# Kernel optimization log

Hardware: AMD Instinct MI355X
Metric: run time of the kernel (lower is better)

## Reference

```python
import jax, jax.numpy as jnp
import numpy as np

N_HEAD = 16
N_EMBD = 1024
B, T = 4, 1024


def setup_inputs() -> dict:
    key = jax.random.key(0)
    ks = jax.random.split(key, 8)
    hs = N_EMBD // N_HEAD
    x = jax.random.normal(ks[0], (B, T, N_EMBD), dtype=jnp.float32)
    # previous-layer attention load per token, ~O(1/T) like a softmax column mean
    refractory_state = jax.random.uniform(ks[1], (B, T), dtype=jnp.float32) / T
    s_attn = 1.0 / np.sqrt(N_EMBD)
    W_attn = jax.random.normal(ks[2], (N_EMBD, 3 * N_EMBD), dtype=jnp.float32) * s_attn
    b_attn = jnp.zeros((3 * N_EMBD,), dtype=jnp.float32)
    W_proj = jax.random.normal(ks[3], (N_EMBD, N_EMBD), dtype=jnp.float32) * s_attn
    b_proj = jnp.zeros((N_EMBD,), dtype=jnp.float32)
    # learnable LIF params, init per module (lif_mode='refractory')
    threshold = jnp.full((N_HEAD,), 0.01, dtype=jnp.float32)
    leak = jnp.full((N_HEAD,), 2.0, dtype=jnp.float32)
    steepness = jnp.full((N_HEAD,), 2.0, dtype=jnp.float32)
    ref_strength = jnp.full((N_HEAD,), -2.0, dtype=jnp.float32)
    cross_w = jnp.full((N_HEAD,), -2.0, dtype=jnp.float32)
    return {
        "x": x, "refractory_state": refractory_state,
        "W_attn": W_attn, "b_attn": b_attn,
        "W_proj": W_proj, "b_proj": b_proj,
        "threshold": threshold, "leak": leak, "steepness": steepness,
        "ref_strength": ref_strength, "cross_w": cross_w,
    }


def reference(x, refractory_state, W_attn, b_attn, W_proj, b_proj,
              threshold, leak, steepness, ref_strength, cross_w):
    Bq, Tq, C = x.shape
    H = N_HEAD
    hs = C // H
    qkv = x @ W_attn + b_attn                     # [B,T,3C]
    q, k, v = jnp.split(qkv, 3, axis=-1)
    q = q.reshape(Bq, Tq, H, hs).transpose(0, 2, 1, 3)  # [B,H,T,hs]
    k = k.reshape(Bq, Tq, H, hs).transpose(0, 2, 1, 3)
    v = v.reshape(Bq, Tq, H, hs).transpose(0, 2, 1, 3)

    att = jnp.einsum('bhqd,bhkd->bhqk', q, k) * (1.0 / jnp.sqrt(jnp.asarray(hs, x.dtype)))
    causal = jnp.tril(jnp.ones((Tq, Tq), dtype=bool))
    att = jnp.where(causal[None, None], att, -jnp.inf)
    probs = jax.nn.softmax(att, axis=-1)          # [B,H,T,T]

    thr = (jnp.abs(threshold) * 0.1)[None, :, None, None]
    lk = jax.nn.sigmoid(leak)[None, :, None, None]
    st = jax.nn.softplus(steepness)[None, :, None, None]
    # refractory: column load over queries + cross-layer load
    column_load = probs.mean(axis=-2, keepdims=True)          # [B,H,1,T]
    eff_thr = thr + jax.nn.softplus(ref_strength)[None, :, None, None] * column_load
    eff_thr = eff_thr + jax.nn.sigmoid(cross_w)[None, :, None, None] * refractory_state[:, None, None, :]

    fire = jax.nn.sigmoid(st * (probs - eff_thr))
    lif_w = fire + lk * (1.0 - fire)
    mod = probs * lif_w
    mod = mod / (mod.sum(axis=-1, keepdims=True) + 1e-8)
    new_refractory = mod.mean(axis=1).mean(axis=-2)           # [B,T]

    y = jnp.einsum('bhqk,bhkd->bhqd', mod, v)
    y = y.transpose(0, 2, 1, 3).reshape(Bq, Tq, C)
    y = y @ W_proj + b_proj
    return y, new_refractory
```

## Files before the change

kernel.cpp:

```cpp
#include <hip/hip_runtime.h>
#include <math.h>

#define B_  4
#define T_  1024
#define C_  1024
#define H_  16
#define HS_ 64
#define K2E 0.1803368801f
#define LOG2E 1.44269504f

typedef _Float16 f16;
typedef _Float16 f16x8 __attribute__((ext_vector_type(8)));
typedef _Float16 f16x4 __attribute__((ext_vector_type(4)));
typedef float f32x4 __attribute__((ext_vector_type(4)));

#define MFMA16(a,b,c) __builtin_amdgcn_mfma_f32_16x16x32_f16(a,b,c,0,0,0)
#define EXP2(x) __builtin_amdgcn_exp2f(x)
#define RCP(x)  __builtin_amdgcn_rcpf(x)

#define PSTRIDE_BH 557056

__device__ __forceinline__ float qsum_(float v){
    v += __shfl_xor(v,1,64); v += __shfl_xor(v,2,64);
    v += __shfl_xor(v,4,64); v += __shfl_xor(v,8,64);
    return v;
}
__device__ __forceinline__ float sigmoidf_(float x){ return 1.0f/(1.0f + __expf(-x)); }
__device__ __forceinline__ float softplusf_(float x){ return fmaxf(x, 0.0f) + log1pf(__expf(-fabsf(x))); }

__device__ __forceinline__ void gload_lds16(const f16* g, f16* l){
    __builtin_amdgcn_global_load_lds(
        (__attribute__((address_space(1))) void*)(void*)g,
        (__attribute__((address_space(3))) void*)(void*)l, 16, 0, 0);
}

__global__ __launch_bounds__(256) void prep_k(
    const float* __restrict__ x, const float* __restrict__ Wa,
    const float* __restrict__ Wp,
    f16* __restrict__ x_h, f16* __restrict__ WaT, f16* __restrict__ WpT,
    float* __restrict__ zbase)
{
    __shared__ float tl[32][33];
    const int bid = blockIdx.x, tid = threadIdx.x;
    if (bid < 2048){
        int i = bid*256 + tid;
        const float4* p = (const float4*)x + (size_t)i*2;
        float4 a = p[0], b = p[1];
        f16x8 o;
        o[0]=(f16)a.x; o[1]=(f16)a.y; o[2]=(f16)a.z; o[3]=(f16)a.w;
        o[4]=(f16)b.x; o[5]=(f16)b.y; o[6]=(f16)b.z; o[7]=(f16)b.w;
        *((f16x8*)x_h + i) = o;
    } else if (bid < 5120){
        int t = bid - 2048;
        int n0 = (t % 96)*32, k0 = (t / 96)*32;
        const int c = tid & 31, r4 = tid >> 5;
        #pragma unroll
        for (int i=0;i<4;i++){ int r = r4*4+i; tl[r][c] = Wa[(size_t)(k0+r)*3072 + n0 + c]; }
        __syncthreads();
        #pragma unroll
        for (int i=0;i<4;i++){ int r = r4*4+i; WaT[(size_t)(n0+r)*1024 + k0 + c] = (f16)tl[c][r]; }
    } else if (bid < 6144){
        int t = bid - 5120;
        int n0 = (t & 31)*32, k0 = (t >> 5)*32;
        const int c = tid & 31, r4 = tid >> 5;
        #pragma unroll
        for (int i=0;i<4;i++){ int r = r4*4+i; tl[r][c] = Wp[(size_t)(k0+r)*1024 + n0 + c]; }
        __syncthreads();
        #pragma unroll
        for (int i=0;i<4;i++){ int r = r4*4+i; WpT[(size_t)(n0+r)*1024 + k0 + c] = (f16)tl[c][r]; }
    } else {
        int idx = (bid - 6144)*256 + tid;
        float4 z; z.x=0.f; z.y=0.f; z.z=0.f; z.w=0.f;
        ((float4*)zbase)[idx] = z;
    }
}

#define CT_STRIDE 132
__global__ __launch_bounds__(256) void gemm_qkv_k(
    const f16* __restrict__ A, const f16* __restrict__ Bt,
    const float* __restrict__ bias,
    f16* __restrict__ Qh, f16* __restrict__ Kh, f16* __restrict__ Vt)
{
    __shared__ __align__(16) f16 smem[16896];
    const int tid = threadIdx.x;
    const int lane = tid & 63, wave = tid >> 6;
    const int lx = lane & 15, quad = lane >> 4;
    const int wm = wave & 1, wn = wave >> 1;
    const int lin = blockIdx.y*24 + blockIdx.x;
    const int nb  = (lin & 7)*96 + (lin >> 3);
    const int m0 = (nb/24)*128, n0 = (nb%24)*128;
    const f16* Ap = A  + (size_t)m0*1024;
    const f16* Bp = Bt + (size_t)n0*1024;
    f32x4 acc[4][4];
    #pragma unroll
    for (int i=0;i<4;i++){
        #pragma unroll
        for (int j=0;j<4;j++){ acc[i][j][0]=0.f;acc[i][j][1]=0.f;acc[i][j][2]=0.f;acc[i][j][3]=0.f; }
    }
#define GQ_STAGE(BUF, KT) { \
    const int k0s = (KT)*32; \
    for (int i=0;i<2;i++){ int c=i*4+wave; \
        gload_lds16(Ap + (size_t)(c*16+lx)*1024 + k0s + quad*8, &smem[(BUF) + c*512]); \
        gload_lds16(Bp + (size_t)(c*16+lx)*1024 + k0s + quad*8, &smem[(BUF) + 4096 + c*512]); } }
#define GQ_COMP(BUF) { \
    f16x8 af[4], bf[4]; \
    for (int mt=0;mt<4;mt++) af[mt] = *(const f16x8*)&smem[(BUF) + (wm*4+mt)*512 + quad*128 + lx*8]; \
    for (int nt=0;nt<4;nt++) bf[nt] = *(const f16x8*)&smem[(BUF) + 4096 + (wn*4+nt)*512 + quad*128 + lx*8]; \
    for (int mt=0;mt<4;mt++) \
        for (int nt=0;nt<4;nt++) \
            acc[mt][nt] = MFMA16(af[mt], bf[nt], acc[mt][nt]); }

    GQ_STAGE(0, 0);
    __syncthreads();
    #pragma unroll 1
    for (int it=0; it<32; it+=2){
        if (it+1 < 32) GQ_STAGE(8192, it+1);
        GQ_COMP(0);
        __syncthreads();
        if (it+2 < 32) GQ_STAGE(0, it+2);
        GQ_COMP(8192);
        __syncthreads();
    }
    f16* Ct = smem;
    #pragma unroll
    for (int mt=0;mt<4;mt++){
        #pragma unroll
        for (int nt=0;nt<4;nt++){
            int n_loc = wn*64 + nt*16 + lx;
            float bv = bias[n0 + n_loc];
            #pragma unroll
            for (int r=0;r<4;r++){
                int m_loc = wm*64 + mt*16 + quad*4 + r;
                Ct[m_loc*CT_STRIDE + n_loc] = (f16)(acc[mt][nt][r] + bv);
            }
        }
    }
    __syncthreads();
    const int bb = m0 >> 10;
    if (n0 < 2048){
        for (int it=0; it<8; it++){
            int row = it*32 + wave*8 + (lane>>3);
            int ch  = lane & 7;
            int m_loc = row >> 1, half = row & 1;
            f16x8 v = *(const f16x8*)&Ct[m_loc*CT_STRIDE + half*64 + ch*8];
            int n = n0 + half*64;
            int which = n >> 10, cc = n & 1023, h = cc >> 6;
            int t = (m0 + m_loc) & 1023;
            f16* dst = (which==0) ? Qh : Kh;
            *(f16x8*)(dst + ((size_t)(bb*16+h)*1024 + t)*64 + ch*8) = v;
        }
    } else {
        for (int it=0; it<8; it++){
            int drow = it*16 + wave*4 + (lane>>4);
            int ch   = lane & 15;
            int cc = (n0 + drow) & 1023;
            int h = cc >> 6, d = cc & 63;
            f16 tmp[8];
            #pragma unroll
            for (int j=0;j<8;j++) tmp[j] = Ct[(ch*8+j)*CT_STRIDE + drow];
            int t = (m0 + ch*8) & 1023;
            *(f16x8*)(Vt + ((size_t)(bb*16+h)*64 + d)*1024 + t) = *(f16x8*)tmp;
        }
    }
}

__global__ __launch_bounds__(256) void gemm_proj_k(
    const f16* __restrict__ A, const f16* __restrict__ Bt,
    const float* __restrict__ bias, float* __restrict__ out,
    const float* __restrict__ racc)
{
    if (blockIdx.x == 512){
        float* oref = out + (size_t)B_*T_*C_;
        #pragma unroll
        for (int j=0;j<16;j++){
            int idx = j*256 + threadIdx.x;
            oref[idx] = racc[idx] * (1.0f/(H_*T_));
        }
        return;
    }
    __shared__ __align__(16) f16 smem[12288];
    const int tid = threadIdx.x;
    const int lane = tid & 63, wave = tid >> 6;
    const int lx = lane & 15, quad = lane >> 4;
    const int wm = wave & 1, wn = wave >> 1;
    const int lin = blockIdx.x;
    const int nb  = (lin & 7)*64 + (lin >> 3);
    const int m0 = (nb >> 4)*128, n0 = (nb & 15)*64;
    const f16* Ap = A  + (size_t)m0*1024;
    const f16* Bp = Bt + (size_t)n0*1024;
    f32x4 acc[4][2];
    #pragma unroll
    for (int i=0;i<4;i++){
        #pragma unroll
        for (int j=0;j<2;j++){ acc[i][j][0]=0.f;acc[i][j][1]=0.f;acc[i][j][2]=0.f;acc[i][j][3]=0.f; }
    }
#define GP_STAGE(BUF, KT) { \
    const int k0s = (KT)*32; \
    for (int i=0;i<2;i++){ int c=i*4+wave; \
        gload_lds16(Ap + (size_t)(c*16+lx)*1024 + k0s + quad*8, &smem[(BUF) + c*512]); } \
    gload_lds16(Bp + (size_t)(wave*16+lx)*1024 + k0s + quad*8, &smem[(BUF) + 4096 + wave*512]); }
#define GP_COMP(BUF) { \
    f16x8 af[4], bf[2]; \
    for (int mt=0;mt<4;mt++) af[mt] = *(const f16x8*)&smem[(BUF) + (wm*4+mt)*512 + quad*128 + lx*8]; \
    for (int nt=0;nt<2;nt++) bf[nt] = *(const f16x8*)&smem[(BUF) + 4096 + (wn*2+nt)*512 + quad*128 + lx*8]; \
    for (int mt=0;mt<4;mt++) \
        for (int nt=0;nt<2;nt++) \
            acc[mt][nt] = MFMA16(af[mt], bf[nt], acc[mt][nt]); }

    GP_STAGE(0, 0);
    __syncthreads();
    #pragma unroll 1
    for (int it=0; it<32; it+=2){
        if (it+1 < 32) GP_STAGE(6144, it+1);
        GP_COMP(0);
        __syncthreads();
        if (it+2 < 32) GP_STAGE(0, it+2);
        GP_COMP(6144);
        __syncthreads();
    }
    #pragma unroll
    for (int mt=0;mt<4;mt++){
        #pragma unroll
        for (int nt=0;nt<2;nt++){
            int n = n0 + wn*32 + nt*16 + lx;
            float bv = bias[n];
            #pragma unroll
            for (int r=0;r<4;r++){
                int m = m0 + wm*64 + mt*16 + quad*4 + r;
                out[(size_t)m*1024 + n] = acc[mt][nt][r] + bv;
            }
        }
    }
}

__global__ __launch_bounds__(256) void attn_stats_k(
    const f16* __restrict__ Qh, const f16* __restrict__ Kh,
    float* __restrict__ rowl, float* __restrict__ colp,
    f16* __restrict__ Pbuf)
{
    __shared__ __align__(16) f16 Kl[8192];
    __shared__ __align__(16) f16 Pl[4][16*72];
    __shared__ float invl_sh[64];
    const int tid = threadIdx.x;
    const int lane = tid & 63, wave = tid >> 6;
    const int lx = lane & 15, quad = lane >> 4;
    const int g  = 15 - (blockIdx.x >> 6);
    const int bh = blockIdx.x & 63;
    const int qpos = wave*16 + quad*4;
    const size_t kbase = (size_t)bh*65536;
    const int S = (g+1)*64;
    f16* __restrict__ Pblk = Pbuf + (size_t)bh*PSTRIDE_BH + (size_t)4096*((g*(g+1))>>1);

    const size_t qoff = ((size_t)bh*1024 + g*64 + wave*16 + lx)*64;
    f16x8 aq0 = *(const f16x8*)(Qh + qoff + quad*8);
    f16x8 aq1 = *(const f16x8*)(Qh + qoff + 32 + quad*8);

#define KLOAD(dst, KT) { \
    for (int i=0;i<2;i++){ int u=i*4+wave, cc=u&3, kh=u>>2; \
        dst[i] = *(const f16x8*)(Kh + kbase + (size_t)((KT)*64 + cc*16+lx)*64 + kh*32 + quad*8); } }
#define KSTORE(src, BUF) { \
    for (int i=0;i<2;i++){ int u=i*4+wave, cc=u&3, kh=u>>2; \
        *(f16x8*)&Kl[(BUF) + cc*1024 + kh*512 + quad*128 + lx*8] = src[i]; } }
#define STATS1_TILE(KT, BUF) { \
    const bool diag = ((KT) == g); \
    for (int nt=0;nt<4;nt++){ \
        f32x4 sc = {0.f,0.f,0.f,0.f}; \
        f16x8 b0 = *(const f16x8*)&Kl[(BUF) + nt*1024 + quad*128 + lx*8]; \
        f16x8 b1 = *(const f16x8*)&Kl[(BUF) + nt*1024 + 512 + quad*128 + lx*8]; \
        sc = MFMA16(aq0, b0, sc); \
        sc = MFMA16(aq1, b1, sc); \
        for (int r=0;r<4;r++){ \
            float sv = sc[r]; \
            if (diag && (nt*16+lx) > (qpos + r)) sv = -1e4f; \
            float p = EXP2(sv*K2E); \
            ls[r] += p; \
            Pl[wave][(quad*4+r)*72 + nt*16 + lx] = (f16)p; \
        } } \
    for (int it2=0; it2<2; it2++){ \
        int qq = it2*8 + (lane>>3), chh = lane & 7; \
        f16x8 v = *(const f16x8*)&Pl[wave][qq*72 + chh*8]; \
        *(f16x8*)(Pblk + (size_t)(wave*16+qq)*S + (KT)*64 + chh*8) = v; } }

    f16x8 rkE[2], rkO[2];
    float ls[4] = {0.f,0.f,0.f,0.f};
    KLOAD(rkE, 0);
    KSTORE(rkE, 0);
    if (g >= 1) KLOAD(rkO, 1);
    __syncthreads();
    #pragma unroll 1
    for (int kt=0; kt<=g; kt+=2){
        if (kt+2 <= g) KLOAD(rkE, kt+2);
        if (kt+1 <= g) KSTORE(rkO, 4096);
        STATS1_TILE(kt, 0);
        __syncthreads();
        if (kt+1 <= g){
            if (kt+3 <= g) KLOAD(rkO, kt+3);
            if (kt+2 <= g) KSTORE(rkE, 0);
            STATS1_TILE(kt+1, 4096);
            __syncthreads();
        }
    }
    #pragma unroll
    for (int r=0;r<4;r++){
        float l = qsum_(ls[r]);
        if (lx == 0){
            rowl[(size_t)bh*1024 + g*64 + qpos + r] = l;
            invl_sh[qpos + r] = RCP(l);
        }
    }
    __syncthreads();
    if (tid < (g+1)*16){
        const int k0 = tid*4;
        float a0=0.f, a1=0.f, a2=0.f, a3=0.f;
        const f16* pr = Pblk + k0;
        #pragma unroll 4
        for (int q=0;q<64;q++){
            f16x4 v = *(const f16x4*)(pr + (size_t)q*S);
            float w = invl_sh[q];
            a0 += (float)v[0]*w; a1 += (float)v[1]*w;
            a2 += (float)v[2]*w; a3 += (float)v[3]*w;
        }
        float* cp = colp + (size_t)bh*1024 + k0;
        atomicAdd(cp+0,a0); atomicAdd(cp+1,a1);
        atomicAdd(cp+2,a2); atomicAdd(cp+3,a3);
    }
}

__global__ __launch_bounds__(256) void attn_apply_k(
    const f16* __restrict__ Vt,
    const float* __restrict__ rowl,
    const float* __restrict__ colp, const float* __restrict__ refr,
    const float* __restrict__ threshold, const float* __restrict__ leak,
    const float* __restrict__ steepness, const float* __restrict__ ref_strength,
    const float* __restrict__ cross_w,
    f16* __restrict__ Yh, float* __restrict__ racc,
    f16* __restrict__ Pbuf)
{
    __shared__ __align__(16) f16 Pl[4][16*72];
    __shared__ float eb[1024];
    __shared__ float invl_sh[64];
    __shared__ float invD_sh[64];
    const int tid = threadIdx.x;
    const int lane = tid & 63, wave = tid >> 6;
    const int lx = lane & 15, quad = lane >> 4;
    const int g  = 15 - (blockIdx.x >> 6);
    const int bh = blockIdx.x & 63;
    const int b  = bh >> 4, h = bh & 15;
    const size_t kbase = (size_t)bh*65536;
    const int S = (g+1)*64;
    f16* __restrict__ Pblk = Pbuf + (size_t)bh*PSTRIDE_BH + (size_t)4096*((g*(g+1))>>1);

    const float thr = fabsf(threshold[h])*0.1f;
    const float lk  = sigmoidf_(leak[h]);
    const float st2 = softplusf_(steepness[h]) * LOG2E;
    const float sprT= softplusf_(ref_strength[h]) * (1.0f/T_);
    const float cw  = sigmoidf_(cross_w[h]);
    const float Alk = 1.f - lk;

    {
        float4 cp = *(const float4*)(colp + (size_t)bh*1024 + tid*4);
        float4 rf = *(const float4*)(refr + (size_t)b*1024 + tid*4);
        eb[tid*4+0] = st2*(thr + sprT*cp.x + cw*rf.x);
        eb[tid*4+1] = st2*(thr + sprT*cp.y + cw*rf.y);
        eb[tid*4+2] = st2*(thr + sprT*cp.z + cw*rf.z);
        eb[tid*4+3] = st2*(thr + sprT*cp.w + cw*rf.w);
    }
    if (tid < 64) invl_sh[tid] = RCP(rowl[(size_t)bh*1024 + g*64 + tid]);
    __syncthreads();

    const float wli = invl_sh[wave*16 + lx];

    f32x4 y[4];
    #pragma unroll
    for (int i=0;i<4;i++){ y[i][0]=0.f;y[i][1]=0.f;y[i][2]=0.f;y[i][3]=0.f; }
    float Dp = 0.f;

#define PLOADX(dst, KT) { \
    const f16* pp = Pblk + (size_t)(wave*16 + lx)*S + (KT)*64 + quad*8; \
    dst[0] = *(const f16x8*)(pp); \
    dst[1] = *(const f16x8*)(pp + 32); }
#define RVLOAD(dst, KT) { \
    for (int dt=0;dt<4;dt++){ \
        const f16* vp = Vt + kbase + (size_t)(dt*16 + lx)*1024 + (KT)*64 + quad*8; \
        dst[dt*2]   = *(const f16x8*)(vp); \
        dst[dt*2+1] = *(const f16x8*)(vp + 32); } }
#define LIF_TILE(KT, pv, af0, af1) { \
    const float* ebp = &eb[(KT)*64 + quad*8]; \
    float4 eA0 = *(const float4*)(ebp); \
    float4 eA1 = *(const float4*)(ebp+4); \
    float4 eB0 = *(const float4*)(ebp+32); \
    float4 eB1 = *(const float4*)(ebp+36); \
    float ea[8] = {eA0.x,eA0.y,eA0.z,eA0.w,eA1.x,eA1.y,eA1.z,eA1.w}; \
    float ebb[8] = {eB0.x,eB0.y,eB0.z,eB0.w,eB1.x,eB1.y,eB1.z,eB1.w}; \
    for (int jj=0;jj<8;jj++){ \
        float p = (float)pv[0][jj] * wli; \
        float fire = RCP(1.f + EXP2(ea[jj] - st2*p)); \
        float pw = p*(lk + Alk*fire); \
        Dp += pw; af0[jj] = (f16)pw; } \
    for (int jj=0;jj<8;jj++){ \
        float p = (float)pv[1][jj] * wli; \
        float fire = RCP(1.f + EXP2(ebb[jj] - st2*p)); \
        float pw = p*(lk + Alk*fire); \
        Dp += pw; af1[jj] = (f16)pw; } }
#define MFMA8(af0, af1, rv) { \
    __builtin_amdgcn_s_setprio(1); \
    for (int dt=0;dt<4;dt++){ \
        y[dt] = MFMA16(af0, rv[dt*2],   y[dt]); \
        y[dt] = MFMA16(af1, rv[dt*2+1], y[dt]); } \
    __builtin_amdgcn_s_setprio(0); }

    f16x8 rvA[8], rvB[8], pvA[2], pvB[2], af0, af1;
    PLOADX(pvA, 0); RVLOAD(rvA, 0);
    if (g >= 1){ PLOADX(pvB, 1); RVLOAD(rvB, 1); }
    #pragma unroll 1
    for (int kt=0; kt<=g; kt+=2){
        LIF_TILE(kt, pvA, af0, af1);
        if (kt+2 <= g) PLOADX(pvA, kt+2);
        MFMA8(af0, af1, rvA);
        if (kt+2 <= g) RVLOAD(rvA, kt+2);
        if (kt+1 <= g){
            LIF_TILE(kt+1, pvB, af0, af1);
            if (kt+3 <= g) PLOADX(pvB, kt+3);
            MFMA8(af0, af1, rvB);
            if (kt+3 <= g) RVLOAD(rvB, kt+3);
        }
    }
    Dp += __shfl_xor(Dp,16,64); Dp += __shfl_xor(Dp,32,64);
    float invDl = RCP(Dp + 1e-8f);
    if (quad == 0) invD_sh[wave*16 + lx] = invDl;

    float invD[4];
    #pragma unroll
    for (int r=0;r<4;r++) invD[r] = invD_sh[wave*16 + quad*4 + r];
    #pragma unroll
    for (int dt=0;dt<4;dt++){
        #pragma unroll
        for (int r=0;r<4;r++)
            Pl[wave][(quad*4+r)*72 + dt*16 + lx] = (f16)(y[dt][r]*invD[r]);
    }
    #pragma unroll
    for (int it=0; it<2; it++){
        int q = it*8 + (lane>>3), ch = lane & 7;
        f16x8 v = *(const f16x8*)&Pl[wave][q*72 + ch*8];
        *(f16x8*)(Yh + (size_t)(b*1024 + g*64 + wave*16 + q)*1024 + h*64 + ch*8) = v;
    }

    __syncthreads();

    if (tid < (g+1)*16){
        const int k0 = tid*4;
        float4 ebv = *(const float4*)&eb[k0];
        float a0=0.f, a1=0.f, a2=0.f, a3=0.f;
        const f16* pr = Pblk + k0;
        #pragma unroll 4
        for (int q=0;q<64;q++){
            f16x4 v = *(const f16x4*)(pr + (size_t)q*S);
            float wl = invl_sh[q], wd = invD_sh[q];
            float p0 = (float)v[0]*wl, p1 = (float)v[1]*wl;
            float p2 = (float)v[2]*wl, p3 = (float)v[3]*wl;
            float f0 = RCP(1.f + EXP2(ebv.x - st2*p0));
            float f1 = RCP(1.f + EXP2(ebv.y - st2*p1));
            float f2 = RCP(1.f + EXP2(ebv.z - st2*p2));
            float f3 = RCP(1.f + EXP2(ebv.w - st2*p3));
            a0 += p0*(lk + Alk*f0)*wd; a1 += p1*(lk + Alk*f1)*wd;
            a2 += p2*(lk + Alk*f2)*wd; a3 += p3*(lk + Alk*f3)*wd;
        }
        float* rp = racc + (size_t)b*1024 + k0;
        atomicAdd(rp+0,a0); atomicAdd(rp+1,a1);
        atomicAdd(rp+2,a2); atomicAdd(rp+3,a3);
    }
}

extern "C" void kernel_launch(void* const* d_in, const int* in_sizes, int n_in,
                              void* d_out, int out_size, void* d_ws, size_t ws_size,
                              hipStream_t stream) {
    (void)in_sizes; (void)n_in; (void)out_size; (void)ws_size;
    const float* x           = (const float*)d_in[0];
    const float* refr        = (const float*)d_in[1];
    const float* W_attn      = (const float*)d_in[2];
    const float* b_attn      = (const float*)d_in[3];
    const float* W_proj      = (const float*)d_in[4];
    const float* b_proj      = (const float*)d_in[5];
    const float* threshold   = (const float*)d_in[6];
    const float* leak        = (const float*)d_in[7];
    const float* steepness   = (const float*)d_in[8];
    const float* ref_strength= (const float*)d_in[9];
    const float* cross_w     = (const float*)d_in[10];
    float* out = (float*)d_out;

    char* ws = (char*)d_ws;
    f16* x_h = (f16*)ws;                       ws += (size_t)4096*1024*2;
    f16* WaT = (f16*)ws;                       ws += (size_t)3072*1024*2;
    f16* WpT = (f16*)ws;                       ws += (size_t)1024*1024*2;
    f16* Qh  = (f16*)ws;                       ws += (size_t)64*1024*64*2;
    f16* Kh  = (f16*)ws;                       ws += (size_t)64*1024*64*2;
    f16* Vt  = (f16*)ws;                       ws += (size_t)64*64*1024*2;
    f16* Yh  = (f16*)ws;                       ws += (size_t)4096*1024*2;
    float* rowl = (float*)ws;                  ws += (size_t)65536*4;
    float* colp = (float*)ws;                  ws += (size_t)65536*4;
    float* racc = (float*)ws;                  ws += (size_t)4096*4;
    f16* Pbuf = (f16*)ws;                      ws += (size_t)64*PSTRIDE_BH*2;

    prep_k<<<dim3(6212), dim3(256), 0, stream>>>(x, W_attn, W_proj, x_h, WaT, WpT, colp);
    gemm_qkv_k<<<dim3(24,32), dim3(256), 0, stream>>>(x_h, WaT, b_attn, Qh, Kh, Vt);
    attn_stats_k<<<dim3(1024), dim3(256), 0, stream>>>(Qh, Kh, rowl, colp, Pbuf);
    attn_apply_k<<<dim3(1024), dim3(256), 0, stream>>>(
        Vt, rowl, colp, refr,
        threshold, leak, steepness, ref_strength, cross_w, Yh, racc, Pbuf);
    gemm_proj_k<<<dim3(513), dim3(256), 0, stream>>>(Yh, WpT, b_proj, out, racc);
}
```

Measured before the change: 277.0 us.

## Stage V tiles in shared memory once per block instead of per-wave global loads

The attention-apply kernel previously had each of the four waves load the full 64x64 V tile from global memory into registers. Now each wave loads a quarter of the tile, writes it into a double-buffered LDS array, and all waves read their MFMA B operands from LDS. This cuts redundant global/L2 traffic for V by four and reduces register pressure. In exchange it adds __syncthreads barriers per tile and LDS read traffic, and it drops the setprio hints around the MFMAs.

```diff
diff --git a/kernel.cpp b/kernel.cpp
--- a/kernel.cpp
+++ b/kernel.cpp
@@ -336,6 +336,7 @@
     f16* __restrict__ Yh, float* __restrict__ racc,
     f16* __restrict__ Pbuf)
 {
+    __shared__ __align__(16) f16 Vl[8192];
     __shared__ __align__(16) f16 Pl[4][16*72];
     __shared__ float eb[1024];
     __shared__ float invl_sh[64];
@@ -375,16 +376,17 @@
     for (int i=0;i<4;i++){ y[i][0]=0.f;y[i][1]=0.f;y[i][2]=0.f;y[i][3]=0.f; }
     float Dp = 0.f;
 
+#define VLOAD(dst, KT) { \
+    for (int i=0;i<2;i++){ int u=i*4+wave, cc=u&3, kh=u>>2; \
+        dst[i] = *(const f16x8*)(Vt + kbase + (size_t)(cc*16+lx)*1024 + (KT)*64 + kh*32 + quad*8); } }
+#define VSTORE(src, BUF) { \
+    for (int i=0;i<2;i++){ int u=i*4+wave, cc=u&3, kh=u>>2; \
+        *(f16x8*)&Vl[(BUF) + cc*1024 + kh*512 + quad*128 + lx*8] = src[i]; } }
 #define PLOADX(dst, KT) { \
     const f16* pp = Pblk + (size_t)(wave*16 + lx)*S + (KT)*64 + quad*8; \
     dst[0] = *(const f16x8*)(pp); \
     dst[1] = *(const f16x8*)(pp + 32); }
-#define RVLOAD(dst, KT) { \
-    for (int dt=0;dt<4;dt++){ \
-        const f16* vp = Vt + kbase + (size_t)(dt*16 + lx)*1024 + (KT)*64 + quad*8; \
-        dst[dt*2]   = *(const f16x8*)(vp); \
-        dst[dt*2+1] = *(const f16x8*)(vp + 32); } }
-#define LIF_TILE(KT, pv, af0, af1) { \
+#define APPLY_T(KT, BUF, pv) { \
     const float* ebp = &eb[(KT)*64 + quad*8]; \
     float4 eA0 = *(const float4*)(ebp); \
     float4 eA1 = *(const float4*)(ebp+4); \
@@ -392,6 +394,7 @@
     float4 eB1 = *(const float4*)(ebp+36); \
     float ea[8] = {eA0.x,eA0.y,eA0.z,eA0.w,eA1.x,eA1.y,eA1.z,eA1.w}; \
     float ebb[8] = {eB0.x,eB0.y,eB0.z,eB0.w,eB1.x,eB1.y,eB1.z,eB1.w}; \
+    f16x8 af0, af1; \
     for (int jj=0;jj<8;jj++){ \
         float p = (float)pv[0][jj] * wli; \
         float fire = RCP(1.f + EXP2(ea[jj] - st2*p)); \
@@ -401,33 +404,35 @@
         float p = (float)pv[1][jj] * wli; \
         float fire = RCP(1.f + EXP2(ebb[jj] - st2*p)); \
         float pw = p*(lk + Alk*fire); \
-        Dp += pw; af1[jj] = (f16)pw; } }
-#define MFMA8(af0, af1, rv) { \
-    __builtin_amdgcn_s_setprio(1); \
+        Dp += pw; af1[jj] = (f16)pw; } \
     for (int dt=0;dt<4;dt++){ \
-        y[dt] = MFMA16(af0, rv[dt*2],   y[dt]); \
-        y[dt] = MFMA16(af1, rv[dt*2+1], y[dt]); } \
-    __builtin_amdgcn_s_setprio(0); }
-
-    f16x8 rvA[8], rvB[8], pvA[2], pvB[2], af0, af1;
-    PLOADX(pvA, 0); RVLOAD(rvA, 0);
-    if (g >= 1){ PLOADX(pvB, 1); RVLOAD(rvB, 1); }
+        f16x8 bv0 = *(const f16x8*)&Vl[(BUF) + dt*1024 + quad*128 + lx*8]; \
+        f16x8 bv1 = *(const f16x8*)&Vl[(BUF) + dt*1024 + 512 + quad*128 + lx*8]; \
+        y[dt] = MFMA16(af0, bv0, y[dt]); \
+        y[dt] = MFMA16(af1, bv1, y[dt]); } }
+
+    f16x8 rvE[2], rvO[2], pvE[2], pvO[2];
+    VLOAD(rvE, 0); PLOADX(pvE, 0);
+    VSTORE(rvE, 0);
+    if (g >= 1){ VLOAD(rvO, 1); PLOADX(pvO, 1); }
+    __syncthreads();
     #pragma unroll 1
     for (int kt=0; kt<=g; kt+=2){
-        LIF_TILE(kt, pvA, af0, af1);
-        if (kt+2 <= g) PLOADX(pvA, kt+2);
-        MFMA8(af0, af1, rvA);
-        if (kt+2 <= g) RVLOAD(rvA, kt+2);
+        if (kt+2 <= g) VLOAD(rvE, kt+2);
+        if (kt+1 <= g) VSTORE(rvO, 4096);
+        APPLY_T(kt, 0, pvE);
+        if (kt+2 <= g) PLOADX(pvE, kt+2);
+        __syncthreads();
         if (kt+1 <= g){
-            LIF_TILE(kt+1, pvB, af0, af1);
-            if (kt+3 <= g) PLOADX(pvB, kt+3);
-            MFMA8(af0, af1, rvB);
-            if (kt+3 <= g) RVLOAD(rvB, kt+3);
+            if (kt+3 <= g) VLOAD(rvO, kt+3);
+            if (kt+2 <= g) VSTORE(rvE, 0);
+            APPLY_T(kt+1, 4096, pvO);
+            if (kt+3 <= g) PLOADX(pvO, kt+3);
+            __syncthreads();
         }
     }
     Dp += __shfl_xor(Dp,16,64); Dp += __shfl_xor(Dp,32,64);
-    float invDl = RCP(Dp + 1e-8f);
-    if (quad == 0) invD_sh[wave*16 + lx] = invDl;
+    if (quad == 0) invD_sh[wave*16 + lx] = RCP(Dp + 1e-8f);
 
     float invD[4];
     #pragma unroll
```

Measured after the change: 261.1 us. 5.7% less time.
